# Optimization experiments

Hardware: AMD Instinct MI355X
Metric: run time of the kernel (lower is better)

The kernel has to match this reference:

```python
import jax, jax.numpy as jnp
import numpy as np

N = 50000      # nodes
E = 800000     # edges (before self-loops)
F_IN = 128     # num_features
HID = 32       # hidden_channels
HEADS = 4
CLS = 40       # num_classes
NEG_SLOPE = 0.2


def setup_inputs() -> dict:
    key = jax.random.key(0)
    ks = jax.random.split(key, 10)
    s = 0.1
    x = jax.random.normal(ks[0], (N, F_IN), jnp.float32)
    edge_index = jax.random.randint(ks[1], (2, E), 0, N, jnp.int32)
    W1 = jax.random.normal(ks[2], (F_IN, HEADS * HID), jnp.float32) * s
    att_src1 = jax.random.normal(ks[3], (HEADS, HID), jnp.float32) * s
    att_dst1 = jax.random.normal(ks[4], (HEADS, HID), jnp.float32) * s
    b1 = jnp.zeros((HEADS * HID,), jnp.float32)
    W2 = jax.random.normal(ks[5], (HEADS * HID, CLS), jnp.float32) * s
    att_src2 = jax.random.normal(ks[6], (1, CLS), jnp.float32) * s
    att_dst2 = jax.random.normal(ks[7], (1, CLS), jnp.float32) * s
    b2 = jnp.zeros((CLS,), jnp.float32)
    return {"x": x, "edge_index": edge_index,
            "W1": W1, "att_src1": att_src1, "att_dst1": att_dst1, "b1": b1,
            "W2": W2, "att_src2": att_src2, "att_dst2": att_dst2, "b2": b2}


def gat_layer(x, src, dst, W, a_src, a_dst, b, concat):
    """PyG GATConv: per-head linear, edge attention logits a_src.h_j + a_dst.h_i,
    LeakyReLU, segment softmax over incoming edges per dst, weighted scatter-sum."""
    n = x.shape[0]
    H, C = a_src.shape
    h = (x @ W).reshape(n, H, C)                       # [N, H, C]
    al_s = jnp.einsum('nhc,hc->nh', h, a_src)          # [N, H]
    al_d = jnp.einsum('nhc,hc->nh', h, a_dst)          # [N, H]
    e = jax.nn.leaky_relu(al_s[src] + al_d[dst], NEG_SLOPE)  # [E, H]
    e_max = jax.lax.stop_gradient(jax.ops.segment_max(e, dst, num_segments=n))
    e = jnp.exp(e - e_max[dst])
    denom = jax.ops.segment_sum(e, dst, num_segments=n)      # [N, H]
    alpha = e / (denom[dst] + 1e-16)                         # [E, H]
    out = jax.ops.segment_sum(h[src] * alpha[:, :, None], dst, num_segments=n)  # [N, H, C]
    out = out.reshape(n, H * C) if concat else out.mean(axis=1)
    return out + b


def reference(x, edge_index, W1, att_src1, att_dst1, b1, W2, att_src2, att_dst2, b2):
    n = x.shape[0]
    loops = jnp.arange(n, dtype=edge_index.dtype)
    src = jnp.concatenate([edge_index[0], loops])  # PyG adds self-loops by default
    dst = jnp.concatenate([edge_index[1], loops])
    h = gat_layer(x, src, dst, W1, att_src1, att_dst1, b1, concat=True)
    h = jax.nn.relu(h)  # dropout is identity in eval mode
    h = gat_layer(h, src, dst, W2, att_src2, att_dst2, b2, concat=False)
    return jax.nn.log_softmax(h, axis=1)
```

## Files before the change

### kernel.cpp

```cpp
#include <hip/hip_runtime.h>
#include <hip/hip_bf16.h>
#include <cstdint>
#include <cstddef>

#define NN 50000
#define EE 800000
#define FIN 128
#define D1 128
#define HEADS 4
#define HID 32
#define CLS 40
#define NEG 0.2f
#define MAXDEG 64
#define P2 128
#define PSZ2 391
#define CAP 8192
#define ABLK 400
#define ASLICE 500
#define GEMM1B 391

typedef __attribute__((ext_vector_type(8))) short short8;
typedef __attribute__((ext_vector_type(4))) float float4v;

union U16 { uint4 u; short8 s; };

__device__ __forceinline__ float bf2f(unsigned short u) {
    union { unsigned int i; float f; } v; v.i = ((unsigned int)u) << 16; return v.f;
}
__device__ __forceinline__ unsigned short f2bf(float f) {
    union { unsigned int i; float f; } v; v.f = f;
    unsigned int r = v.i + 0x7fffu + ((v.i >> 16) & 1u);
    return (unsigned short)(r >> 16);
}

__global__ __launch_bounds__(256) void bucket_k(const int* __restrict__ eidx,
                                                unsigned int* __restrict__ seg,
                                                int* __restrict__ seg_cnt) {
    __shared__ int hist[P2], base_s[P2], run[P2];
    int t = threadIdx.x;
    if (t < P2) { hist[t] = 0; run[t] = 0; }
    __syncthreads();
    const int4* dst4 = (const int4*)(eidx + EE);
    const int4* src4 = (const int4*)eidx;
    int i0 = blockIdx.x * ASLICE;
    for (int i = i0 + t; i < i0 + ASLICE; i += 256) {
        int4 d = dst4[i];
        atomicAdd(&hist[d.x / PSZ2], 1);
        atomicAdd(&hist[d.y / PSZ2], 1);
        atomicAdd(&hist[d.z / PSZ2], 1);
        atomicAdd(&hist[d.w / PSZ2], 1);
    }
    __syncthreads();
    if (t < P2) base_s[t] = (hist[t] > 0) ? atomicAdd(&seg_cnt[t], hist[t]) : 0;
    __syncthreads();
    for (int i = i0 + t; i < i0 + ASLICE; i += 256) {
        int4 d = dst4[i];
        int4 s = src4[i];
        int p, off, idx;
        p = d.x / PSZ2; off = atomicAdd(&run[p], 1); idx = base_s[p] + off;
        if (idx < CAP) seg[(size_t)p * CAP + idx] = ((unsigned)s.x << 16) | (unsigned)(d.x - p * PSZ2);
        p = d.y / PSZ2; off = atomicAdd(&run[p], 1); idx = base_s[p] + off;
        if (idx < CAP) seg[(size_t)p * CAP + idx] = ((unsigned)s.y << 16) | (unsigned)(d.y - p * PSZ2);
        p = d.z / PSZ2; off = atomicAdd(&run[p], 1); idx = base_s[p] + off;
        if (idx < CAP) seg[(size_t)p * CAP + idx] = ((unsigned)s.z << 16) | (unsigned)(d.z - p * PSZ2);
        p = d.w / PSZ2; off = atomicAdd(&run[p], 1); idx = base_s[p] + off;
        if (idx < CAP) seg[(size_t)p * CAP + idx] = ((unsigned)s.w << 16) | (unsigned)(d.w - p * PSZ2);
    }
}

union BSM {
    struct { uint4 Wl[2048]; float sas[128]; float sad[128]; } g;
    int hist[PSZ2];
};

__global__ __launch_bounds__(256, 4) void bg_k(const unsigned int* __restrict__ seg,
                                               const int* __restrict__ seg_cnt,
                                               int* __restrict__ cnt,
                                               unsigned short* __restrict__ ssrcp,
                                               const float* __restrict__ X,
                                               const float* __restrict__ W,
                                               const float* __restrict__ as1,
                                               const float* __restrict__ ad1,
                                               unsigned int* __restrict__ H1b,
                                               float* __restrict__ ALS1,
                                               float* __restrict__ ALD1) {
    __shared__ BSM sm;
    int t = threadIdx.x;

    if (blockIdx.x < P2) {
        int p = blockIdx.x;
        int lo = p * PSZ2;
        int psz = min(PSZ2, NN - lo);
        for (int i = t; i < psz; i += 256) {
            sm.hist[i] = 1;
            ssrcp[(size_t)(lo + i) * MAXDEG] = (unsigned short)(lo + i);
        }
        __syncthreads();
        int m = min(seg_cnt[p], CAP);
        const unsigned int* sp = seg + (size_t)p * CAP;
        for (int i = t; i < m; i += 256) {
            unsigned int pr = sp[i];
            int dl  = (int)(pr & 0xffffu);
            int src = (int)(pr >> 16);
            int slot = atomicAdd(&sm.hist[dl], 1);
            if (slot < MAXDEG) ssrcp[(size_t)(lo + dl) * MAXDEG + slot] = (unsigned short)src;
        }
        __syncthreads();
        for (int i = t; i < psz; i += 256) cnt[lo + i] = sm.hist[i];
        return;
    }

    int bI = blockIdx.x - P2;
    if (t < 128) { sm.g.sas[t] = as1[t]; sm.g.sad[t] = ad1[t]; }
    for (int g = t; g < 2048; g += 256) {
        int ct = g >> 8, rem = g & 255, kc = rem >> 6, l = rem & 63;
        int c = ct * 16 + (l & 15);
        int k0 = kc * 32 + (l >> 4) * 8;
        U16 u;
#pragma unroll
        for (int j = 0; j < 8; j++) u.s[j] = (short)f2bf(W[(k0 + j) * D1 + c]);
        sm.g.Wl[g] = u.u;
    }
    __syncthreads();

    int wid = t >> 6, lane = t & 63, quad = lane >> 4, lrow = lane & 15;
    int wrow0 = bI * 128 + wid * 32;

    short8 afr[2][4];
#pragma unroll
    for (int rt = 0; rt < 2; rt++) {
        int r = wrow0 + rt * 16 + lrow;
#pragma unroll
        for (int kc = 0; kc < 4; kc++) {
            short8 a = {0, 0, 0, 0, 0, 0, 0, 0};
            if (r < NN) {
                const float* xp = X + (size_t)r * FIN + kc * 32 + quad * 8;
                float4 x0 = *(const float4*)xp;
                float4 x1 = *(const float4*)(xp + 4);
                a[0] = (short)f2bf(x0.x); a[1] = (short)f2bf(x0.y);
                a[2] = (short)f2bf(x0.z); a[3] = (short)f2bf(x0.w);
                a[4] = (short)f2bf(x1.x); a[5] = (short)f2bf(x1.y);
                a[6] = (short)f2bf(x1.z); a[7] = (short)f2bf(x1.w);
            }
            afr[rt][kc] = a;
        }
    }

    float4v acc[2][4];

    for (int cp = 0; cp < 2; ++cp) {
#pragma unroll
        for (int rt = 0; rt < 2; rt++)
#pragma unroll
            for (int c4 = 0; c4 < 4; c4++) acc[rt][c4] = (float4v)(0.f);

#pragma unroll
        for (int c4 = 0; c4 < 4; c4++) {
#pragma unroll
            for (int kc = 0; kc < 4; kc++) {
                U16 b; b.u = sm.g.Wl[((cp * 4 + c4) * 4 + kc) * 64 + lane];
                acc[0][c4] = __builtin_amdgcn_mfma_f32_16x16x32_bf16(afr[0][kc], b.s, acc[0][c4], 0, 0, 0);
                acc[1][c4] = __builtin_amdgcn_mfma_f32_16x16x32_bf16(afr[1][kc], b.s, acc[1][c4], 0, 0, 0);
            }
        }

#pragma unroll
        for (int rt = 0; rt < 2; rt++) {
#pragma unroll
            for (int reg = 0; reg < 4; reg++) {
                float ps[2] = {0.f, 0.f};
                float pd[2] = {0.f, 0.f};
#pragma unroll
                for (int c4 = 0; c4 < 4; c4++) {
                    float v = acc[rt][c4][reg];
                    int ct = cp * 4 + c4;
                    ps[c4 >> 1] += v * sm.g.sas[ct * 16 + lrow];
                    pd[c4 >> 1] += v * sm.g.sad[ct * 16 + lrow];
                }
#pragma unroll
                for (int o = 1; o < 16; o <<= 1) {
#pragma unroll
                    for (int h = 0; h < 2; h++) {
                        ps[h] += __shfl_xor(ps[h], o);
                        pd[h] += __shfl_xor(pd[h], o);
                    }
                }
                int r = wrow0 + rt * 16 + quad * 4 + reg;
                if (lrow == 0 && r < NN) {
                    *(float2*)&ALS1[(size_t)r * 4 + cp * 2] = make_float2(ps[0], ps[1]);
                    *(float2*)&ALD1[(size_t)r * 4 + cp * 2] = make_float2(pd[0], pd[1]);
                }
            }
        }

#pragma unroll
        for (int rt = 0; rt < 2; rt++)
#pragma unroll
            for (int c4 = 0; c4 < 4; c4++)
#pragma unroll
                for (int reg = 0; reg < 4; reg++) {
                    float v = acc[rt][c4][reg];
                    float o = __shfl_xor(v, 1);
                    int r = wrow0 + rt * 16 + quad * 4 + reg;
                    if (((lane & 1) == 0) && r < NN) {
                        unsigned int u = (unsigned int)f2bf(v) | ((unsigned int)f2bf(o) << 16);
                        H1b[(size_t)r * 64 + (cp * 4 + c4) * 8 + (lrow >> 1)] = u;
                    }
                }
    }
}

__global__ __launch_bounds__(256) void gather1_k(const int* __restrict__ cnt,
                                                 const unsigned short* __restrict__ ssrcp,
                                                 const uint4* __restrict__ H1b4,
                                                 const float4* __restrict__ ALS,
                                                 const float4* __restrict__ ALD,
                                                 const float* __restrict__ b1,
                                                 uint4* __restrict__ OUT1b4) {
    __shared__ float wlds[4][MAXDEG][4];
    __shared__ int sidlds[4][MAXDEG];
    int wid = threadIdx.x >> 6, lane = threadIdx.x & 63;
    int v = blockIdx.x * 4 + wid;
    int deg = min(cnt[v], MAXDEG);
    float4 ad = ALD[v];
    float w0 = 0.f, w1 = 0.f, w2 = 0.f, w3 = 0.f;
    if (lane < deg) {
        int s = (int)ssrcp[(size_t)v * MAXDEG + lane];
        sidlds[wid][lane] = s;
        float4 as = ALS[s];
        float l0 = as.x + ad.x; l0 = l0 > 0.f ? l0 : NEG * l0;
        float l1 = as.y + ad.y; l1 = l1 > 0.f ? l1 : NEG * l1;
        float l2 = as.z + ad.z; l2 = l2 > 0.f ? l2 : NEG * l2;
        float l3 = as.w + ad.w; l3 = l3 > 0.f ? l3 : NEG * l3;
        w0 = __expf(l0); w1 = __expf(l1); w2 = __expf(l2); w3 = __expf(l3);
        wlds[wid][lane][0] = w0; wlds[wid][lane][1] = w1;
        wlds[wid][lane][2] = w2; wlds[wid][lane][3] = w3;
    }
    float d0 = w0, d1 = w1, d2 = w2, d3 = w3;
#pragma unroll
    for (int o = 1; o < 64; o <<= 1) {
        d0 += __shfl_xor(d0, o); d1 += __shfl_xor(d1, o);
        d2 += __shfl_xor(d2, o); d3 += __shfl_xor(d3, o);
    }
    __syncthreads();
    int g = lane >> 4, l = lane & 15, head = l >> 2;
    float a0=0.f,a1=0.f,a2=0.f,a3=0.f,a4=0.f,a5=0.f,a6=0.f,a7=0.f;
    {
        int j = g;
        bool valid = j < deg;
        float wj = 0.f; uint4 q = {};
        if (valid) {
            wj = wlds[wid][j][head];
            q = H1b4[(size_t)sidlds[wid][j] * 16 + l];
        }
        while (valid) {
            int jn = j + 4;
            bool vn = jn < deg;
            float wn = 0.f; uint4 qn = {};
            if (vn) {
                wn = wlds[wid][jn][head];
                qn = H1b4[(size_t)sidlds[wid][jn] * 16 + l];
            }
            a0 += wj * bf2f((unsigned short)(q.x & 0xffffu));
            a1 += wj * bf2f((unsigned short)(q.x >> 16));
            a2 += wj * bf2f((unsigned short)(q.y & 0xffffu));
            a3 += wj * bf2f((unsigned short)(q.y >> 16));
            a4 += wj * bf2f((unsigned short)(q.z & 0xffffu));
            a5 += wj * bf2f((unsigned short)(q.z >> 16));
            a6 += wj * bf2f((unsigned short)(q.w & 0xffffu));
            a7 += wj * bf2f((unsigned short)(q.w >> 16));
            j = jn; valid = vn; wj = wn; q = qn;
        }
    }
#pragma unroll
    for (int o = 16; o < 64; o <<= 1) {
        a0 += __shfl_xor(a0, o); a1 += __shfl_xor(a1, o);
        a2 += __shfl_xor(a2, o); a3 += __shfl_xor(a3, o);
        a4 += __shfl_xor(a4, o); a5 += __shfl_xor(a5, o);
        a6 += __shfl_xor(a6, o); a7 += __shfl_xor(a7, o);
    }
    if (lane < 16) {
        float den = (head == 0) ? d0 : (head == 1) ? d1 : (head == 2) ? d2 : d3;
        den += 1e-16f;
        float4 bA = *(const float4*)&b1[8 * l];
        float4 bB = *(const float4*)&b1[8 * l + 4];
        float o0 = fmaxf(a0 / den + bA.x, 0.f);
        float o1 = fmaxf(a1 / den + bA.y, 0.f);
        float o2 = fmaxf(a2 / den + bA.z, 0.f);
        float o3 = fmaxf(a3 / den + bA.w, 0.f);
        float o4 = fmaxf(a4 / den + bB.x, 0.f);
        float o5 = fmaxf(a5 / den + bB.y, 0.f);
        float o6 = fmaxf(a6 / den + bB.z, 0.f);
        float o7 = fmaxf(a7 / den + bB.w, 0.f);
        uint4 u;
        u.x = (unsigned int)f2bf(o0) | ((unsigned int)f2bf(o1) << 16);
        u.y = (unsigned int)f2bf(o2) | ((unsigned int)f2bf(o3) << 16);
        u.z = (unsigned int)f2bf(o4) | ((unsigned int)f2bf(o5) << 16);
        u.w = (unsigned int)f2bf(o6) | ((unsigned int)f2bf(o7) << 16);
        OUT1b4[(size_t)v * 16 + l] = u;
    }
}

__global__ __launch_bounds__(256) void gemm2_k(const unsigned int* __restrict__ OUT1b,
                                               const float* __restrict__ W2,
                                               const float* __restrict__ as2,
                                               const float* __restrict__ ad2,
                                               unsigned int* __restrict__ H2b,
                                               float* __restrict__ ALS2,
                                               float* __restrict__ ALD2) {
    __shared__ uint4 Wl[768];
    __shared__ float sas[48], sad[48];
    int t = threadIdx.x;
    if (t < 48) {
        sas[t] = (t < CLS) ? as2[t] : 0.f;
        sad[t] = (t < CLS) ? ad2[t] : 0.f;
    }
    for (int g = t; g < 768; g += 256) {
        int ct = g >> 8, rem = g & 255, kc = rem >> 6, l = rem & 63;
        int c = ct * 16 + (l & 15);
        int k0 = kc * 32 + (l >> 4) * 8;
        U16 u;
#pragma unroll
        for (int j = 0; j < 8; j++)
            u.s[j] = (c < CLS) ? (short)f2bf(W2[(k0 + j) * CLS + c]) : (short)0;
        Wl[g] = u.u;
    }
    __syncthreads();

    int wid = t >> 6, lane = t & 63, quad = lane >> 4, lrow = lane & 15;
    int wrow0 = blockIdx.x * 128 + wid * 32;

    U16 afr[2][4];
#pragma unroll
    for (int rt = 0; rt < 2; rt++) {
        int r = wrow0 + rt * 16 + lrow;
#pragma unroll
        for (int kc = 0; kc < 4; kc++) {
            if (r < NN)
                afr[rt][kc].u = ((const uint4*)OUT1b)[(size_t)r * 16 + kc * 4 + quad];
            else
                afr[rt][kc].u = make_uint4(0, 0, 0, 0);
        }
    }

    float4v acc[2][3];
#pragma unroll
    for (int rt = 0; rt < 2; rt++)
#pragma unroll
        for (int ct = 0; ct < 3; ct++) acc[rt][ct] = (float4v)(0.f);

#pragma unroll
    for (int ct = 0; ct < 3; ct++) {
#pragma unroll
        for (int kc = 0; kc < 4; kc++) {
            U16 b; b.u = Wl[(ct * 4 + kc) * 64 + lane];
            acc[0][ct] = __builtin_amdgcn_mfma_f32_16x16x32_bf16(afr[0][kc].s, b.s, acc[0][ct], 0, 0, 0);
            acc[1][ct] = __builtin_amdgcn_mfma_f32_16x16x32_bf16(afr[1][kc].s, b.s, acc[1][ct], 0, 0, 0);
        }
    }

#pragma unroll
    for (int rt = 0; rt < 2; rt++) {
#pragma unroll
        for (int reg = 0; reg < 4; reg++) {
            float ps = 0.f, pd = 0.f;
#pragma unroll
            for (int ct = 0; ct < 3; ct++) {
                float v = acc[rt][ct][reg];
                ps += v * sas[ct * 16 + lrow];
                pd += v * sad[ct * 16 + lrow];
            }
#pragma unroll
            for (int o = 1; o < 16; o <<= 1) {
                ps += __shfl_xor(ps, o);
                pd += __shfl_xor(pd, o);
            }
            int r = wrow0 + rt * 16 + quad * 4 + reg;
            if (lrow == 0 && r < NN) {
                ALS2[r] = ps;
                ALD2[r] = pd;
            }
        }
    }

#pragma unroll
    for (int rt = 0; rt < 2; rt++)
#pragma unroll
        for (int ct = 0; ct < 3; ct++)
#pragma unroll
            for (int reg = 0; reg < 4; reg++) {
                float v = acc[rt][ct][reg];
                float o = __shfl_xor(v, 1);
                int r = wrow0 + rt * 16 + quad * 4 + reg;
                int c = ct * 16 + lrow;
                if (((lane & 1) == 0) && c < CLS && r < NN) {
                    unsigned int u = (unsigned int)f2bf(v) | ((unsigned int)f2bf(o) << 16);
                    H2b[(size_t)r * 20 + (c >> 1)] = u;
                }
            }
}

__global__ __launch_bounds__(256) void gather2_k(const int* __restrict__ cnt,
                                                 const unsigned short* __restrict__ ssrcp,
                                                 const unsigned int* __restrict__ H2b,
                                                 const float* __restrict__ ALS,
                                                 const float* __restrict__ ALD,
                                                 const float* __restrict__ b2,
                                                 float* __restrict__ out) {
    int wid = threadIdx.x >> 6, t = threadIdx.x & 63;
    int v = blockIdx.x * 4 + wid;
    int deg = min(cnt[v], MAXDEG);
    __shared__ float w[4][MAXDEG];
    __shared__ int sid[4][MAXDEG];
    __shared__ float part[4][3][CLS];
    float den = 0.f;
    float adv = ALD[v];
    if (t < deg) {
        int s = (int)ssrcp[(size_t)v * MAXDEG + t];
        sid[wid][t] = s;
        float l = ALS[s] + adv; l = l > 0.f ? l : NEG * l;
        float e = __expf(l);
        w[wid][t] = e; den = e;
    }
    __syncthreads();
    int g = t / 20, c = t % 20;
    if (t < 60) {
        float ax = 0.f, ay = 0.f;
        int j = g;
        bool valid = j < deg;
        float wj = 0.f; unsigned int u = 0u;
        if (valid) { wj = w[wid][j]; u = H2b[(size_t)sid[wid][j] * 20 + c]; }
        while (valid) {
            int jn = j + 3;
            bool vn = jn < deg;
            float wn = 0.f; unsigned int un = 0u;
            if (vn) { wn = w[wid][jn]; un = H2b[(size_t)sid[wid][jn] * 20 + c]; }
            ax += wj * bf2f((unsigned short)(u & 0xffffu));
            ay += wj * bf2f((unsigned short)(u >> 16));
            j = jn; valid = vn; wj = wn; u = un;
        }
        part[wid][g][2 * c] = ax;
        part[wid][g][2 * c + 1] = ay;
    }
#pragma unroll
    for (int o = 32; o > 0; o >>= 1) den += __shfl_xor(den, o);
    __syncthreads();
    float z = (t < CLS) ? (part[wid][0][t] + part[wid][1][t] + part[wid][2][t]) / (den + 1e-16f) + b2[t]
                        : -1e30f;
    float mx = z;
#pragma unroll
    for (int o = 32; o > 0; o >>= 1) mx = fmaxf(mx, __shfl_xor(mx, o));
    float ex = (t < CLS) ? __expf(z - mx) : 0.f;
    float se = ex;
#pragma unroll
    for (int o = 32; o > 0; o >>= 1) se += __shfl_xor(se, o);
    if (t < CLS) out[(size_t)v * CLS + t] = z - mx - __logf(se);
}

extern "C" void kernel_launch(void* const* d_in, const int* in_sizes, int n_in,
                              void* d_out, int out_size, void* d_ws, size_t ws_size,
                              hipStream_t stream) {
    const float* x   = (const float*)d_in[0];
    const int*   eix = (const int*)d_in[1];
    const float* W1  = (const float*)d_in[2];
    const float* as1 = (const float*)d_in[3];
    const float* ad1 = (const float*)d_in[4];
    const float* b1  = (const float*)d_in[5];
    const float* W2  = (const float*)d_in[6];
    const float* as2 = (const float*)d_in[7];
    const float* ad2 = (const float*)d_in[8];
    const float* b2  = (const float*)d_in[9];
    float* out = (float*)d_out;

    char* p = (char*)d_ws;
    auto carve = [&](size_t bytes) -> void* {
        void* r = (void*)p;
        p += (bytes + 255) & ~(size_t)255;
        return r;
    };
    unsigned int* H1b   = (unsigned int*)carve((size_t)NN * 64 * 4);
    unsigned int* OUT1b = (unsigned int*)carve((size_t)NN * 64 * 4);
    unsigned int* H2b   = (unsigned int*)carve((size_t)NN * 20 * 4);
    float* ALS1 = (float*)carve((size_t)NN * 4 * 4);
    float* ALD1 = (float*)carve((size_t)NN * 4 * 4);
    float* ALS2 = (float*)carve((size_t)NN * 4);
    float* ALD2 = (float*)carve((size_t)NN * 4);
    int* cnt    = (int*)carve((size_t)NN * 4);
    unsigned short* ssrcp = (unsigned short*)carve((size_t)NN * MAXDEG * 2);
    unsigned int* seg   = (unsigned int*)carve((size_t)P2 * CAP * 4);
    int* seg_cnt        = (int*)carve((size_t)P2 * 4);

    hipMemsetAsync(seg_cnt, 0, (size_t)P2 * 4, stream);

    bucket_k<<<ABLK, 256, 0, stream>>>(eix, seg, seg_cnt);
    bg_k<<<P2 + GEMM1B, 256, 0, stream>>>(seg, seg_cnt, cnt, ssrcp, x, W1, as1, ad1,
                                          H1b, ALS1, ALD1);
    gather1_k<<<NN / 4, 256, 0, stream>>>(cnt, ssrcp, (const uint4*)H1b,
                                          (const float4*)ALS1, (const float4*)ALD1,
                                          b1, (uint4*)OUT1b);
    gemm2_k<<<(NN + 127) / 128, 256, 0, stream>>>(OUT1b, W2, as2, ad2, H2b, ALS2, ALD2);
    gather2_k<<<NN / 4, 256, 0, stream>>>(cnt, ssrcp, H2b, ALS2, ALD2, b2, out);
}
```

Baseline: 206.1 us.

## Use per-block bucket slots and head-major H1 layout with per-head gather

Each bucket block now writes edges into private fixed-capacity slots per partition, which removes the histogram pass, the global atomic offset reservation and the memset. The scatter kernel scans all slots and masks by each block's count. The layer-1 features are stored head-major, so gather1 processes one head at a time with 4 lanes per row and 16 edges in parallel. The aim is better cache locality per head. In exchange it adds four sequential passes with block syncs, drops the software prefetch, and reads a larger, sparsely filled slot array.

```diff
diff --git a/kernel.cpp b/kernel.cpp
--- a/kernel.cpp
+++ b/kernel.cpp
@@ -14,9 +14,9 @@
 #define MAXDEG 64
 #define P2 128
 #define PSZ2 391
-#define CAP 8192
 #define ABLK 400
 #define ASLICE 500
+#define CAPB 64
 #define GEMM1B 391
 
 typedef __attribute__((ext_vector_type(8))) short short8;
@@ -35,46 +35,39 @@
 
 __global__ __launch_bounds__(256) void bucket_k(const int* __restrict__ eidx,
                                                 unsigned int* __restrict__ seg,
-                                                int* __restrict__ seg_cnt) {
-    __shared__ int hist[P2], base_s[P2], run[P2];
+                                                int* __restrict__ blk_cnt) {
+    __shared__ int run[P2];
     int t = threadIdx.x;
-    if (t < P2) { hist[t] = 0; run[t] = 0; }
+    if (t < P2) run[t] = 0;
     __syncthreads();
     const int4* dst4 = (const int4*)(eidx + EE);
     const int4* src4 = (const int4*)eidx;
-    int i0 = blockIdx.x * ASLICE;
-    for (int i = i0 + t; i < i0 + ASLICE; i += 256) {
-        int4 d = dst4[i];
-        atomicAdd(&hist[d.x / PSZ2], 1);
-        atomicAdd(&hist[d.y / PSZ2], 1);
-        atomicAdd(&hist[d.z / PSZ2], 1);
-        atomicAdd(&hist[d.w / PSZ2], 1);
-    }
-    __syncthreads();
-    if (t < P2) base_s[t] = (hist[t] > 0) ? atomicAdd(&seg_cnt[t], hist[t]) : 0;
-    __syncthreads();
+    int b = blockIdx.x;
+    int i0 = b * ASLICE;
     for (int i = i0 + t; i < i0 + ASLICE; i += 256) {
         int4 d = dst4[i];
         int4 s = src4[i];
-        int p, off, idx;
-        p = d.x / PSZ2; off = atomicAdd(&run[p], 1); idx = base_s[p] + off;
-        if (idx < CAP) seg[(size_t)p * CAP + idx] = ((unsigned)s.x << 16) | (unsigned)(d.x - p * PSZ2);
-        p = d.y / PSZ2; off = atomicAdd(&run[p], 1); idx = base_s[p] + off;
-        if (idx < CAP) seg[(size_t)p * CAP + idx] = ((unsigned)s.y << 16) | (unsigned)(d.y - p * PSZ2);
-        p = d.z / PSZ2; off = atomicAdd(&run[p], 1); idx = base_s[p] + off;
-        if (idx < CAP) seg[(size_t)p * CAP + idx] = ((unsigned)s.z << 16) | (unsigned)(d.z - p * PSZ2);
-        p = d.w / PSZ2; off = atomicAdd(&run[p], 1); idx = base_s[p] + off;
-        if (idx < CAP) seg[(size_t)p * CAP + idx] = ((unsigned)s.w << 16) | (unsigned)(d.w - p * PSZ2);
-    }
+        int p, off;
+        p = d.x / PSZ2; off = atomicAdd(&run[p], 1);
+        if (off < CAPB) seg[((size_t)p * ABLK + b) * CAPB + off] = ((unsigned)s.x << 16) | (unsigned)(d.x - p * PSZ2);
+        p = d.y / PSZ2; off = atomicAdd(&run[p], 1);
+        if (off < CAPB) seg[((size_t)p * ABLK + b) * CAPB + off] = ((unsigned)s.y << 16) | (unsigned)(d.y - p * PSZ2);
+        p = d.z / PSZ2; off = atomicAdd(&run[p], 1);
+        if (off < CAPB) seg[((size_t)p * ABLK + b) * CAPB + off] = ((unsigned)s.z << 16) | (unsigned)(d.z - p * PSZ2);
+        p = d.w / PSZ2; off = atomicAdd(&run[p], 1);
+        if (off < CAPB) seg[((size_t)p * ABLK + b) * CAPB + off] = ((unsigned)s.w << 16) | (unsigned)(d.w - p * PSZ2);
+    }
+    __syncthreads();
+    if (t < P2) blk_cnt[(size_t)t * ABLK + b] = min(run[t], CAPB);
 }
 
 union BSM {
     struct { uint4 Wl[2048]; float sas[128]; float sad[128]; } g;
-    int hist[PSZ2];
+    struct { int hist[PSZ2]; int bcnt[ABLK]; } b;
 };
 
 __global__ __launch_bounds__(256, 4) void bg_k(const unsigned int* __restrict__ seg,
-                                               const int* __restrict__ seg_cnt,
+                                               const int* __restrict__ blk_cnt,
                                                int* __restrict__ cnt,
                                                unsigned short* __restrict__ ssrcp,
                                                const float* __restrict__ X,
@@ -92,21 +85,26 @@
         int lo = p * PSZ2;
         int psz = min(PSZ2, NN - lo);
         for (int i = t; i < psz; i += 256) {
-            sm.hist[i] = 1;
+            sm.b.hist[i] = 1;
             ssrcp[(size_t)(lo + i) * MAXDEG] = (unsigned short)(lo + i);
         }
+        for (int i = t; i < ABLK; i += 256)
+            sm.b.bcnt[i] = blk_cnt[(size_t)p * ABLK + i];
         __syncthreads();
-        int m = min(seg_cnt[p], CAP);
-        const unsigned int* sp = seg + (size_t)p * CAP;
-        for (int i = t; i < m; i += 256) {
-            unsigned int pr = sp[i];
-            int dl  = (int)(pr & 0xffffu);
-            int src = (int)(pr >> 16);
-            int slot = atomicAdd(&sm.hist[dl], 1);
-            if (slot < MAXDEG) ssrcp[(size_t)(lo + dl) * MAXDEG + slot] = (unsigned short)src;
+        const unsigned int* sp = seg + (size_t)p * ABLK * CAPB;
+        for (int gI = t; gI < ABLK * CAPB; gI += 256) {
+            int bb = gI >> 6;
+            int i  = gI & (CAPB - 1);
+            if (i < sm.b.bcnt[bb]) {
+                unsigned int pr = sp[gI];
+                int dl  = (int)(pr & 0xffffu);
+                int src = (int)(pr >> 16);
+                int slot = atomicAdd(&sm.b.hist[dl], 1);
+                if (slot < MAXDEG) ssrcp[(size_t)(lo + dl) * MAXDEG + slot] = (unsigned short)src;
+            }
         }
         __syncthreads();
-        for (int i = t; i < psz; i += 256) cnt[lo + i] = sm.hist[i];
+        for (int i = t; i < psz; i += 256) cnt[lo + i] = sm.b.hist[i];
         return;
     }
 
@@ -203,8 +201,9 @@
                     float o = __shfl_xor(v, 1);
                     int r = wrow0 + rt * 16 + quad * 4 + reg;
                     if (((lane & 1) == 0) && r < NN) {
+                        int ct = cp * 4 + c4;
                         unsigned int u = (unsigned int)f2bf(v) | ((unsigned int)f2bf(o) << 16);
-                        H1b[(size_t)r * 64 + (cp * 4 + c4) * 8 + (lrow >> 1)] = u;
+                        H1b[(size_t)(ct >> 1) * (NN * 16) + (size_t)r * 16 + (ct & 1) * 8 + (lrow >> 1)] = u;
                     }
                 }
     }
@@ -213,54 +212,44 @@
 __global__ __launch_bounds__(256) void gather1_k(const int* __restrict__ cnt,
                                                  const unsigned short* __restrict__ ssrcp,
                                                  const uint4* __restrict__ H1b4,
-                                                 const float4* __restrict__ ALS,
-                                                 const float4* __restrict__ ALD,
+                                                 const float* __restrict__ ALS,
+                                                 const float* __restrict__ ALD,
                                                  const float* __restrict__ b1,
                                                  uint4* __restrict__ OUT1b4) {
-    __shared__ float wlds[4][MAXDEG][4];
+    __shared__ float wlds[4][MAXDEG];
     __shared__ int sidlds[4][MAXDEG];
     int wid = threadIdx.x >> 6, lane = threadIdx.x & 63;
     int v = blockIdx.x * 4 + wid;
     int deg = min(cnt[v], MAXDEG);
-    float4 ad = ALD[v];
-    float w0 = 0.f, w1 = 0.f, w2 = 0.f, w3 = 0.f;
-    if (lane < deg) {
-        int s = (int)ssrcp[(size_t)v * MAXDEG + lane];
-        sidlds[wid][lane] = s;
-        float4 as = ALS[s];
-        float l0 = as.x + ad.x; l0 = l0 > 0.f ? l0 : NEG * l0;
-        float l1 = as.y + ad.y; l1 = l1 > 0.f ? l1 : NEG * l1;
-        float l2 = as.z + ad.z; l2 = l2 > 0.f ? l2 : NEG * l2;
-        float l3 = as.w + ad.w; l3 = l3 > 0.f ? l3 : NEG * l3;
-        w0 = __expf(l0); w1 = __expf(l1); w2 = __expf(l2); w3 = __expf(l3);
-        wlds[wid][lane][0] = w0; wlds[wid][lane][1] = w1;
-        wlds[wid][lane][2] = w2; wlds[wid][lane][3] = w3;
-    }
-    float d0 = w0, d1 = w1, d2 = w2, d3 = w3;
-#pragma unroll
-    for (int o = 1; o < 64; o <<= 1) {
-        d0 += __shfl_xor(d0, o); d1 += __shfl_xor(d1, o);
-        d2 += __shfl_xor(d2, o); d3 += __shfl_xor(d3, o);
-    }
-    __syncthreads();
-    int g = lane >> 4, l = lane & 15, head = l >> 2;
-    float a0=0.f,a1=0.f,a2=0.f,a3=0.f,a4=0.f,a5=0.f,a6=0.f,a7=0.f;
-    {
-        int j = g;
-        bool valid = j < deg;
-        float wj = 0.f; uint4 q = {};
-        if (valid) {
-            wj = wlds[wid][j][head];
-            q = H1b4[(size_t)sidlds[wid][j] * 16 + l];
-        }
-        while (valid) {
-            int jn = j + 4;
-            bool vn = jn < deg;
-            float wn = 0.f; uint4 qn = {};
-            if (vn) {
-                wn = wlds[wid][jn][head];
-                qn = H1b4[(size_t)sidlds[wid][jn] * 16 + l];
-            }
+    int g = lane >> 2, sub = lane & 3;
+
+    for (int h = 0; h < HEADS; ++h) {
+        float adh = ALD[(size_t)v * 4 + h];
+        float w = 0.f;
+        if (lane < deg) {
+            int s;
+            if (h == 0) {
+                s = (int)ssrcp[(size_t)v * MAXDEG + lane];
+                sidlds[wid][lane] = s;
+            } else {
+                s = sidlds[wid][lane];
+            }
+            float l = ALS[(size_t)s * 4 + h] + adh;
+            l = l > 0.f ? l : NEG * l;
+            w = __expf(l);
+            wlds[wid][lane] = w;
+        }
+        float den = w;
+#pragma unroll
+        for (int o = 1; o < 64; o <<= 1) den += __shfl_xor(den, o);
+        __syncthreads();
+
+        float a0=0.f,a1=0.f,a2=0.f,a3=0.f,a4=0.f,a5=0.f,a6=0.f,a7=0.f;
+        const uint4* Hs = H1b4 + (size_t)h * (NN * 4);
+        for (int j = g; j < deg; j += 16) {
+            float wj = wlds[wid][j];
+            int  sj = sidlds[wid][j];
+            uint4 q = Hs[(size_t)sj * 4 + sub];
             a0 += wj * bf2f((unsigned short)(q.x & 0xffffu));
             a1 += wj * bf2f((unsigned short)(q.x >> 16));
             a2 += wj * bf2f((unsigned short)(q.y & 0xffffu));
@@ -269,35 +258,34 @@
             a5 += wj * bf2f((unsigned short)(q.z >> 16));
             a6 += wj * bf2f((unsigned short)(q.w & 0xffffu));
             a7 += wj * bf2f((unsigned short)(q.w >> 16));
-            j = jn; valid = vn; wj = wn; q = qn;
-        }
-    }
-#pragma unroll
-    for (int o = 16; o < 64; o <<= 1) {
-        a0 += __shfl_xor(a0, o); a1 += __shfl_xor(a1, o);
-        a2 += __shfl_xor(a2, o); a3 += __shfl_xor(a3, o);
-        a4 += __shfl_xor(a4, o); a5 += __shfl_xor(a5, o);
-        a6 += __shfl_xor(a6, o); a7 += __shfl_xor(a7, o);
-    }
-    if (lane < 16) {
-        float den = (head == 0) ? d0 : (head == 1) ? d1 : (head == 2) ? d2 : d3;
-        den += 1e-16f;
-        float4 bA = *(const float4*)&b1[8 * l];
-        float4 bB = *(const float4*)&b1[8 * l + 4];
-        float o0 = fmaxf(a0 / den + bA.x, 0.f);
-        float o1 = fmaxf(a1 / den + bA.y, 0.f);
-        float o2 = fmaxf(a2 / den + bA.z, 0.f);
-        float o3 = fmaxf(a3 / den + bA.w, 0.f);
-        float o4 = fmaxf(a4 / den + bB.x, 0.f);
-        float o5 = fmaxf(a5 / den + bB.y, 0.f);
-        float o6 = fmaxf(a6 / den + bB.z, 0.f);
-        float o7 = fmaxf(a7 / den + bB.w, 0.f);
-        uint4 u;
-        u.x = (unsigned int)f2bf(o0) | ((unsigned int)f2bf(o1) << 16);
-        u.y = (unsigned int)f2bf(o2) | ((unsigned int)f2bf(o3) << 16);
-        u.z = (unsigned int)f2bf(o4) | ((unsigned int)f2bf(o5) << 16);
-        u.w = (unsigned int)f2bf(o6) | ((unsigned int)f2bf(o7) << 16);
-        OUT1b4[(size_t)v * 16 + l] = u;
+        }
+#pragma unroll
+        for (int o = 4; o < 64; o <<= 1) {
+            a0 += __shfl_xor(a0, o); a1 += __shfl_xor(a1, o);
+            a2 += __shfl_xor(a2, o); a3 += __shfl_xor(a3, o);
+            a4 += __shfl_xor(a4, o); a5 += __shfl_xor(a5, o);
+            a6 += __shfl_xor(a6, o); a7 += __shfl_xor(a7, o);
+        }
+        if (g == 0) {
+            float d = den + 1e-16f;
+            float4 bA = *(const float4*)&b1[h * 32 + sub * 8];
+            float4 bB = *(const float4*)&b1[h * 32 + sub * 8 + 4];
+            float o0 = fmaxf(a0 / d + bA.x, 0.f);
+            float o1 = fmaxf(a1 / d + bA.y, 0.f);
+            float o2 = fmaxf(a2 / d + bA.z, 0.f);
+            float o3 = fmaxf(a3 / d + bA.w, 0.f);
+            float o4 = fmaxf(a4 / d + bB.x, 0.f);
+            float o5 = fmaxf(a5 / d + bB.y, 0.f);
+            float o6 = fmaxf(a6 / d + bB.z, 0.f);
+            float o7 = fmaxf(a7 / d + bB.w, 0.f);
+            uint4 u;
+            u.x = (unsigned int)f2bf(o0) | ((unsigned int)f2bf(o1) << 16);
+            u.y = (unsigned int)f2bf(o2) | ((unsigned int)f2bf(o3) << 16);
+            u.z = (unsigned int)f2bf(o4) | ((unsigned int)f2bf(o5) << 16);
+            u.w = (unsigned int)f2bf(o6) | ((unsigned int)f2bf(o7) << 16);
+            OUT1b4[(size_t)v * 16 + h * 4 + sub] = u;
+        }
+        __syncthreads();
     }
 }
 
@@ -487,17 +475,15 @@
     float* ALD2 = (float*)carve((size_t)NN * 4);
     int* cnt    = (int*)carve((size_t)NN * 4);
     unsigned short* ssrcp = (unsigned short*)carve((size_t)NN * MAXDEG * 2);
-    unsigned int* seg   = (unsigned int*)carve((size_t)P2 * CAP * 4);
-    int* seg_cnt        = (int*)carve((size_t)P2 * 4);
-
-    hipMemsetAsync(seg_cnt, 0, (size_t)P2 * 4, stream);
-
-    bucket_k<<<ABLK, 256, 0, stream>>>(eix, seg, seg_cnt);
-    bg_k<<<P2 + GEMM1B, 256, 0, stream>>>(seg, seg_cnt, cnt, ssrcp, x, W1, as1, ad1,
+    unsigned int* seg   = (unsigned int*)carve((size_t)P2 * ABLK * CAPB * 4);
+    int* blk_cnt        = (int*)carve((size_t)P2 * ABLK * 4);
+
+
+    bucket_k<<<ABLK, 256, 0, stream>>>(eix, seg, blk_cnt);
+    bg_k<<<P2 + GEMM1B, 256, 0, stream>>>(seg, blk_cnt, cnt, ssrcp, x, W1, as1, ad1,
                                           H1b, ALS1, ALD1);
     gather1_k<<<NN / 4, 256, 0, stream>>>(cnt, ssrcp, (const uint4*)H1b,
-                                          (const float4*)ALS1, (const float4*)ALD1,
-                                          b1, (uint4*)OUT1b);
+                                          ALS1, ALD1, b1, (uint4*)OUT1b);
     gemm2_k<<<(NN + 127) / 128, 256, 0, stream>>>(OUT1b, W2, as2, ad2, H2b, ALS2, ALD2);
     gather2_k<<<NN / 4, 256, 0, stream>>>(cnt, ssrcp, H2b, ALS2, ALD2, b2, out);
 }
```

Result: slower. 271.4 us (+31.7%).

## Bucket edges into fixed per-block slots and use packed float2 bf16 accumulation

Applied to the files above, without the earlier changes.

The edge bucketing kernel now writes each block's edges for a partition into a fixed 64-entry slot and records per-block counts. This removes the histogram pass, the global atomic base allocation and the memset. The partition consumer scans all block slots and skips the empty ones, which means more strided reads over a sparser layout and drops edges if any block/partition pair exceeds 64. Separately, the gather loops unpack bf16 pairs into float2 vectors so the compiler can emit packed FMA instructions.

```diff
diff --git a/kernel.cpp b/kernel.cpp
--- a/kernel.cpp
+++ b/kernel.cpp
@@ -14,13 +14,14 @@
 #define MAXDEG 64
 #define P2 128
 #define PSZ2 391
-#define CAP 8192
 #define ABLK 400
 #define ASLICE 500
+#define CAPB 64
 #define GEMM1B 391
 
 typedef __attribute__((ext_vector_type(8))) short short8;
 typedef __attribute__((ext_vector_type(4))) float float4v;
+typedef __attribute__((ext_vector_type(2))) float float2v;
 
 union U16 { uint4 u; short8 s; };
 
@@ -32,49 +33,47 @@
     unsigned int r = v.i + 0x7fffu + ((v.i >> 16) & 1u);
     return (unsigned short)(r >> 16);
 }
+__device__ __forceinline__ float2v up2(unsigned int u) {
+    union { unsigned int i; float f; } lo, hi;
+    lo.i = u << 16; hi.i = u & 0xffff0000u;
+    float2v r; r[0] = lo.f; r[1] = hi.f; return r;
+}
 
 __global__ __launch_bounds__(256) void bucket_k(const int* __restrict__ eidx,
                                                 unsigned int* __restrict__ seg,
-                                                int* __restrict__ seg_cnt) {
-    __shared__ int hist[P2], base_s[P2], run[P2];
+                                                int* __restrict__ blk_cnt) {
+    __shared__ int run[P2];
     int t = threadIdx.x;
-    if (t < P2) { hist[t] = 0; run[t] = 0; }
+    if (t < P2) run[t] = 0;
     __syncthreads();
     const int4* dst4 = (const int4*)(eidx + EE);
     const int4* src4 = (const int4*)eidx;
-    int i0 = blockIdx.x * ASLICE;
-    for (int i = i0 + t; i < i0 + ASLICE; i += 256) {
-        int4 d = dst4[i];
-        atomicAdd(&hist[d.x / PSZ2], 1);
-        atomicAdd(&hist[d.y / PSZ2], 1);
-        atomicAdd(&hist[d.z / PSZ2], 1);
-        atomicAdd(&hist[d.w / PSZ2], 1);
-    }
-    __syncthreads();
-    if (t < P2) base_s[t] = (hist[t] > 0) ? atomicAdd(&seg_cnt[t], hist[t]) : 0;
-    __syncthreads();
+    int b = blockIdx.x;
+    int i0 = b * ASLICE;
     for (int i = i0 + t; i < i0 + ASLICE; i += 256) {
         int4 d = dst4[i];
         int4 s = src4[i];
-        int p, off, idx;
-        p = d.x / PSZ2; off = atomicAdd(&run[p], 1); idx = base_s[p] + off;
-        if (idx < CAP) seg[(size_t)p * CAP + idx] = ((unsigned)s.x << 16) | (unsigned)(d.x - p * PSZ2);
-        p = d.y / PSZ2; off = atomicAdd(&run[p], 1); idx = base_s[p] + off;
-        if (idx < CAP) seg[(size_t)p * CAP + idx] = ((unsigned)s.y << 16) | (unsigned)(d.y - p * PSZ2);
-        p = d.z / PSZ2; off = atomicAdd(&run[p], 1); idx = base_s[p] + off;
-        if (idx < CAP) seg[(size_t)p * CAP + idx] = ((unsigned)s.z << 16) | (unsigned)(d.z - p * PSZ2);
-        p = d.w / PSZ2; off = atomicAdd(&run[p], 1); idx = base_s[p] + off;
-        if (idx < CAP) seg[(size_t)p * CAP + idx] = ((unsigned)s.w << 16) | (unsigned)(d.w - p * PSZ2);
-    }
+        int p, off;
+        p = d.x / PSZ2; off = atomicAdd(&run[p], 1);
+        if (off < CAPB) seg[((size_t)p * ABLK + b) * CAPB + off] = ((unsigned)s.x << 16) | (unsigned)(d.x - p * PSZ2);
+        p = d.y / PSZ2; off = atomicAdd(&run[p], 1);
+        if (off < CAPB) seg[((size_t)p * ABLK + b) * CAPB + off] = ((unsigned)s.y << 16) | (unsigned)(d.y - p * PSZ2);
+        p = d.z / PSZ2; off = atomicAdd(&run[p], 1);
+        if (off < CAPB) seg[((size_t)p * ABLK + b) * CAPB + off] = ((unsigned)s.z << 16) | (unsigned)(d.z - p * PSZ2);
+        p = d.w / PSZ2; off = atomicAdd(&run[p], 1);
+        if (off < CAPB) seg[((size_t)p * ABLK + b) * CAPB + off] = ((unsigned)s.w << 16) | (unsigned)(d.w - p * PSZ2);
+    }
+    __syncthreads();
+    if (t < P2) blk_cnt[(size_t)t * ABLK + b] = min(run[t], CAPB);
 }
 
 union BSM {
     struct { uint4 Wl[2048]; float sas[128]; float sad[128]; } g;
-    int hist[PSZ2];
+    struct { int hist[PSZ2]; int bcnt[ABLK]; } b;
 };
 
 __global__ __launch_bounds__(256, 4) void bg_k(const unsigned int* __restrict__ seg,
-                                               const int* __restrict__ seg_cnt,
+                                               const int* __restrict__ blk_cnt,
                                                int* __restrict__ cnt,
                                                unsigned short* __restrict__ ssrcp,
                                                const float* __restrict__ X,
@@ -92,21 +91,26 @@
         int lo = p * PSZ2;
         int psz = min(PSZ2, NN - lo);
         for (int i = t; i < psz; i += 256) {
-            sm.hist[i] = 1;
+            sm.b.hist[i] = 1;
             ssrcp[(size_t)(lo + i) * MAXDEG] = (unsigned short)(lo + i);
         }
+        for (int i = t; i < ABLK; i += 256)
+            sm.b.bcnt[i] = blk_cnt[(size_t)p * ABLK + i];
         __syncthreads();
-        int m = min(seg_cnt[p], CAP);
-        const unsigned int* sp = seg + (size_t)p * CAP;
-        for (int i = t; i < m; i += 256) {
-            unsigned int pr = sp[i];
-            int dl  = (int)(pr & 0xffffu);
-            int src = (int)(pr >> 16);
-            int slot = atomicAdd(&sm.hist[dl], 1);
-            if (slot < MAXDEG) ssrcp[(size_t)(lo + dl) * MAXDEG + slot] = (unsigned short)src;
+        const unsigned int* sp = seg + (size_t)p * ABLK * CAPB;
+        for (int gI = t; gI < ABLK * CAPB; gI += 256) {
+            int bb = gI >> 6;
+            int i  = gI & (CAPB - 1);
+            if (i < sm.b.bcnt[bb]) {
+                unsigned int pr = sp[gI];
+                int dl  = (int)(pr & 0xffffu);
+                int src = (int)(pr >> 16);
+                int slot = atomicAdd(&sm.b.hist[dl], 1);
+                if (slot < MAXDEG) ssrcp[(size_t)(lo + dl) * MAXDEG + slot] = (unsigned short)src;
+            }
         }
         __syncthreads();
-        for (int i = t; i < psz; i += 256) cnt[lo + i] = sm.hist[i];
+        for (int i = t; i < psz; i += 256) cnt[lo + i] = sm.b.hist[i];
         return;
     }
 
@@ -244,7 +248,7 @@
     }
     __syncthreads();
     int g = lane >> 4, l = lane & 15, head = l >> 2;
-    float a0=0.f,a1=0.f,a2=0.f,a3=0.f,a4=0.f,a5=0.f,a6=0.f,a7=0.f;
+    float2v A0 = {0.f, 0.f}, A1 = {0.f, 0.f}, A2 = {0.f, 0.f}, A3 = {0.f, 0.f};
     {
         int j = g;
         bool valid = j < deg;
@@ -261,17 +265,16 @@
                 wn = wlds[wid][jn][head];
                 qn = H1b4[(size_t)sidlds[wid][jn] * 16 + l];
             }
-            a0 += wj * bf2f((unsigned short)(q.x & 0xffffu));
-            a1 += wj * bf2f((unsigned short)(q.x >> 16));
-            a2 += wj * bf2f((unsigned short)(q.y & 0xffffu));
-            a3 += wj * bf2f((unsigned short)(q.y >> 16));
-            a4 += wj * bf2f((unsigned short)(q.z & 0xffffu));
-            a5 += wj * bf2f((unsigned short)(q.z >> 16));
-            a6 += wj * bf2f((unsigned short)(q.w & 0xffffu));
-            a7 += wj * bf2f((unsigned short)(q.w >> 16));
+            float2v wv = {wj, wj};
+            A0 += wv * up2(q.x);
+            A1 += wv * up2(q.y);
+            A2 += wv * up2(q.z);
+            A3 += wv * up2(q.w);
             j = jn; valid = vn; wj = wn; q = qn;
         }
     }
+    float a0 = A0[0], a1 = A0[1], a2 = A1[0], a3 = A1[1];
+    float a4 = A2[0], a5 = A2[1], a6 = A3[0], a7 = A3[1];
 #pragma unroll
     for (int o = 16; o < 64; o <<= 1) {
         a0 += __shfl_xor(a0, o); a1 += __shfl_xor(a1, o);
@@ -425,7 +428,7 @@
     __syncthreads();
     int g = t / 20, c = t % 20;
     if (t < 60) {
-        float ax = 0.f, ay = 0.f;
+        float2v A = {0.f, 0.f};
         int j = g;
         bool valid = j < deg;
         float wj = 0.f; unsigned int u = 0u;
@@ -435,12 +438,12 @@
             bool vn = jn < deg;
             float wn = 0.f; unsigned int un = 0u;
             if (vn) { wn = w[wid][jn]; un = H2b[(size_t)sid[wid][jn] * 20 + c]; }
-            ax += wj * bf2f((unsigned short)(u & 0xffffu));
-            ay += wj * bf2f((unsigned short)(u >> 16));
+            float2v wv = {wj, wj};
+            A += wv * up2(u);
             j = jn; valid = vn; wj = wn; u = un;
         }
-        part[wid][g][2 * c] = ax;
-        part[wid][g][2 * c + 1] = ay;
+        part[wid][g][2 * c] = A[0];
+        part[wid][g][2 * c + 1] = A[1];
     }
 #pragma unroll
     for (int o = 32; o > 0; o >>= 1) den += __shfl_xor(den, o);
@@ -487,13 +490,12 @@
     float* ALD2 = (float*)carve((size_t)NN * 4);
     int* cnt    = (int*)carve((size_t)NN * 4);
     unsigned short* ssrcp = (unsigned short*)carve((size_t)NN * MAXDEG * 2);
-    unsigned int* seg   = (unsigned int*)carve((size_t)P2 * CAP * 4);
-    int* seg_cnt        = (int*)carve((size_t)P2 * 4);
-
-    hipMemsetAsync(seg_cnt, 0, (size_t)P2 * 4, stream);
-
-    bucket_k<<<ABLK, 256, 0, stream>>>(eix, seg, seg_cnt);
-    bg_k<<<P2 + GEMM1B, 256, 0, stream>>>(seg, seg_cnt, cnt, ssrcp, x, W1, as1, ad1,
+    unsigned int* seg   = (unsigned int*)carve((size_t)P2 * ABLK * CAPB * 4);
+    int* blk_cnt        = (int*)carve((size_t)P2 * ABLK * 4);
+
+
+    bucket_k<<<ABLK, 256, 0, stream>>>(eix, seg, blk_cnt);
+    bg_k<<<P2 + GEMM1B, 256, 0, stream>>>(seg, blk_cnt, cnt, ssrcp, x, W1, as1, ad1,
                                           H1b, ALS1, ALD1);
     gather1_k<<<NN / 4, 256, 0, stream>>>(cnt, ssrcp, (const uint4*)H1b,
                                           (const float4*)ALS1, (const float4*)ALD1,
```

Result: slower. 217.8 us (+5.6%).
